# Kernel optimization log

Hardware: AMD Instinct MI355X
Metric: run time of the kernel (lower is better)

## Reference

```python
import math
import jax, jax.numpy as jnp
import numpy as np

EMBED_DIM = 512
NUM_HEADS = 8
PROJ_DIM = EMBED_DIM // NUM_HEADS
ATTN_WINDOW = 5
HALF_WINDOW = (ATTN_WINDOW - 1) // 2  # 2
ATTN_PARAM = 1.0
ATTN_DISPLACEMENT = 1
# per-head positions: ['center','left','right','center'] repeated to 8 heads (synst repeats short lists)
HEAD_SHIFTS = np.array([0, -ATTN_DISPLACEMENT, ATTN_DISPLACEMENT, 0] * 2, dtype=np.int32)


def _xavier(key, shape):
    fan_in, fan_out = shape[1], shape[0]
    bound = math.sqrt(6.0 / (fan_in + fan_out))
    return jax.random.uniform(key, shape, jnp.float32, -bound, bound)


def setup_inputs() -> dict:
    key = jax.random.key(0)
    k1, k2, k3, k4, k5 = jax.random.split(key, 5)
    B, S, E = 8, 4096, EMBED_DIM
    return {
        "values": jax.random.normal(k1, (B, S, E), jnp.float32),
        "keys": jax.random.normal(k2, (B, S, E), jnp.float32),
        "queries": jax.random.normal(k3, (B, S, E), jnp.float32),
        "input_weights": _xavier(k4, (E, E)),        # value projection (attn_weights=1, non-learned type)
        "out_proj_w": _xavier(k5, (E, E)),           # output_projection.weight (bias=False)
    }


def reference(values, keys, queries, input_weights, out_proj_w):
    # keys/queries are unused by the hard-coded 'normal' attention path (no QK^T)
    B, S, E = values.shape
    H, Dh, hw, W = NUM_HEADS, PROJ_DIM, HALF_WINDOW, ATTN_WINDOW

    # value projection + head split: [B,S,E] -> [B,H,S,Dh]
    v = values @ input_weights.T
    v = v.reshape(B, S, H, Dh).transpose(0, 2, 1, 3)

    # fixed Gaussian filter over relative distances [-hw, hw] (unnormalized pdf, as in the source)
    dist = jnp.arange(-hw, hw + 1, dtype=jnp.float32)
    filt = (1.0 / (ATTN_PARAM * math.sqrt(2.0 * math.pi))) * jnp.exp(-0.5 * (dist / ATTN_PARAM) ** 2)  # [W]

    shifts = jnp.asarray(HEAD_SHIFTS)            # [H] per-head center displacement
    P = hw + int(np.max(np.abs(HEAD_SHIFTS)))    # pad so all gathers are in range
    vp = jnp.pad(v, ((0, 0), (0, 0), (P, P), (0, 0)))  # [B,H,S+2P,Dh]

    h_ar = jnp.arange(H)[:, None]                # [H,1]
    pos = jnp.arange(S)[None, :]                 # [1,S]
    out = jnp.zeros_like(v)
    for j in range(W):                           # tiny fixed window loop (W=5)
        idx = pos + P + shifts[:, None] + (j - hw)   # [H,S]
        out = out + filt[j] * vp[:, h_ar, idx, :]    # [B,H,S,Dh]

    out = out.transpose(0, 2, 1, 3).reshape(B, S, E)
    return out @ out_proj_w.T
```

## Files before the change

kernel.cpp:

```cpp
#include <hip/hip_runtime.h>
#include <hip/hip_bf16.h>
#include <stdint.h>

typedef __bf16 bf16;
typedef __bf16 bf16x8 __attribute__((ext_vector_type(8)));
typedef float  f32x4  __attribute__((ext_vector_type(4)));

#define BM 128
#define BN 128
#define BK 64
#define E  512
#define SB 4112
#define M1 (8 * SB)
#define M2 32768

__device__ __forceinline__ void gl_lds_16(const bf16* g, bf16* l) {
    __builtin_amdgcn_global_load_lds(
        (__attribute__((address_space(1))) void*)g,
        (__attribute__((address_space(3))) void*)l,
        16, 0, 0);
}

__global__ __launch_bounds__(256)
void gemm_bt_bf16(const bf16* __restrict__ A, const bf16* __restrict__ Bm,
                  bf16* __restrict__ C, int M, int N, int K)
{
    __shared__ bf16 As[BM * BK];
    __shared__ bf16 Bs[BN * BK];

    const int tid  = threadIdx.x;
    const int id   = blockIdx.x;
    const int bm   = id >> 2;
    const int bn   = id & 3;
    const int wave = tid >> 6;
    const int lane = tid & 63;
    const int wm   = wave >> 1;
    const int wn   = wave & 1;

    const int srow = tid >> 3;
    const int scol = (((tid & 7) ^ (srow & 7)) << 3);
    const size_t a_off = (size_t)(bm * BM + srow) * K + scol;
    const size_t b_off = (size_t)(bn * BN + srow) * K + scol;
    const int    l_off = tid * 8;

    f32x4 acc[4][4] = {};
    const int fr = lane & 15;
    const int q  = lane >> 4;

    for (int k0 = 0; k0 < K; k0 += BK) {
#pragma unroll
        for (int c = 0; c < 4; ++c) {
            gl_lds_16(A  + a_off + (size_t)(c * 32) * K + k0, As + c * 2048 + l_off);
            gl_lds_16(Bm + b_off + (size_t)(c * 32) * K + k0, Bs + c * 2048 + l_off);
        }
        __syncthreads();

#pragma unroll
        for (int t = 0; t < 2; ++t) {
            bf16x8 af[4], bfr[4];
#pragma unroll
            for (int i = 0; i < 4; ++i) {
                const int Ra = wm * 64 + i * 16 + fr;
                const int Rb = wn * 64 + i * 16 + fr;
                const int c  = t * 4 + q;
                af[i]  = *(const bf16x8*)(As + Ra * BK + ((c ^ (Ra & 7)) << 3));
                bfr[i] = *(const bf16x8*)(Bs + Rb * BK + ((c ^ (Rb & 7)) << 3));
            }
#pragma unroll
            for (int i = 0; i < 4; ++i)
#pragma unroll
                for (int j = 0; j < 4; ++j)
                    acc[i][j] = __builtin_amdgcn_mfma_f32_16x16x32_bf16(af[i], bfr[j], acc[i][j], 0, 0, 0);
        }
        __syncthreads();
    }

    const int crow = (lane >> 4) << 2;
    const int ccol = lane & 15;
    const int row0 = bm * BM + wm * 64 + crow;
    const int col0 = bn * BN + wn * 64 + ccol;
#pragma unroll
    for (int i = 0; i < 4; ++i)
#pragma unroll
        for (int j = 0; j < 4; ++j)
#pragma unroll
            for (int r = 0; r < 4; ++r)
                C[(size_t)(row0 + i * 16 + r) * N + (col0 + j * 16)] = (bf16)acc[i][j][r];
}

__global__ __launch_bounds__(256)
void gemm2_gather(const bf16* __restrict__ P, const bf16* __restrict__ Bm,
                  float* __restrict__ C)
{
    __shared__ bf16 As[BM * BK];
    __shared__ bf16 Bs[BN * BK];

    const int tid  = threadIdx.x;
    const int id   = blockIdx.x;
    const int bm   = id >> 2;
    const int bn   = id & 3;
    const int wave = tid >> 6;
    const int lane = tid & 63;
    const int wm   = wave >> 1;
    const int wn   = wave & 1;

    const int srow = tid >> 3;
    const int scol = (((tid & 7) ^ (srow & 7)) << 3);
    const size_t b_off = (size_t)(bn * BN + srow) * E + scol;
    const int    l_off = tid * 8;

    f32x4 acc[4][4] = {};
    const int fr = lane & 15;
    const int q  = lane >> 4;

    for (int k0 = 0; k0 < E; k0 += BK) {
        const int h3 = (k0 >> 6) & 3;
        const int sh = (h3 == 1) ? -1 : (h3 == 2) ? 1 : 0;
#pragma unroll
        for (int c = 0; c < 4; ++c) {
            const int m = bm * BM + c * 32 + srow;
            const int prow = (m >> 12) * SB + (m & 4095) + 1 + sh;
            gl_lds_16(P  + (size_t)prow * E + k0 + scol,          As + c * 2048 + l_off);
            gl_lds_16(Bm + b_off + (size_t)(c * 32) * E + k0,     Bs + c * 2048 + l_off);
        }
        __syncthreads();

#pragma unroll
        for (int t = 0; t < 2; ++t) {
            bf16x8 af[4], bfr[4];
#pragma unroll
            for (int i = 0; i < 4; ++i) {
                const int Ra = wm * 64 + i * 16 + fr;
                const int Rb = wn * 64 + i * 16 + fr;
                const int c  = t * 4 + q;
                af[i]  = *(const bf16x8*)(As + Ra * BK + ((c ^ (Ra & 7)) << 3));
                bfr[i] = *(const bf16x8*)(Bs + Rb * BK + ((c ^ (Rb & 7)) << 3));
            }
#pragma unroll
            for (int i = 0; i < 4; ++i)
#pragma unroll
                for (int j = 0; j < 4; ++j)
                    acc[i][j] = __builtin_amdgcn_mfma_f32_16x16x32_bf16(af[i], bfr[j], acc[i][j], 0, 0, 0);
        }
        __syncthreads();
    }

    const int crow = (lane >> 4) << 2;
    const int ccol = lane & 15;
    const int row0 = bm * BM + wm * 64 + crow;
    const int col0 = bn * BN + wn * 64 + ccol;
#pragma unroll
    for (int i = 0; i < 4; ++i)
#pragma unroll
        for (int j = 0; j < 4; ++j)
#pragma unroll
            for (int r = 0; r < 4; ++r)
                C[(size_t)(row0 + i * 16 + r) * E + (col0 + j * 16)] = acc[i][j][r];
}

__global__ __launch_bounds__(256)
void prefilter(const float* __restrict__ vals, bf16* __restrict__ vg)
{
    const int tid  = threadIdx.x;
    const int e8   = tid & 63;
    const int gidx = blockIdx.x * 4 + (tid >> 6);
    const int m0   = gidx << 3;
    const int b    = m0 / SB;
    const int r0   = m0 - b * SB;

    const float filt[5] = {0.05399096651318806f, 0.24197072451914337f,
                           0.3989422804014327f,
                           0.24197072451914337f, 0.05399096651318806f};

    float acc[8][8];
#pragma unroll
    for (int t = 0; t < 8; ++t)
#pragma unroll
        for (int d = 0; d < 8; ++d) acc[t][d] = 0.f;

    const float* bbase = vals + (size_t)b * 4096 * E + e8 * 8;
#pragma unroll
    for (int u = 0; u < 12; ++u) {
        const int sp = r0 - 3 + u;
        if (sp >= 0 && sp < 4096) {
            const f32x4* p = (const f32x4*)(bbase + (size_t)sp * E);
            const f32x4 x0 = p[0], x1 = p[1];
            const float x[8] = {x0[0], x0[1], x0[2], x0[3],
                                x1[0], x1[1], x1[2], x1[3]};
#pragma unroll
            for (int t = 0; t < 8; ++t) {
                const int j = u - t;
                if (j >= 0 && j < 5) {
                    const float w = filt[j];
#pragma unroll
                    for (int d = 0; d < 8; ++d) acc[t][d] += w * x[d];
                }
            }
        }
    }
#pragma unroll
    for (int t = 0; t < 8; ++t) {
        bf16x8 o;
#pragma unroll
        for (int d = 0; d < 8; ++d) o[d] = (bf16)acc[t][d];
        *((bf16x8*)vg + (size_t)(m0 + t) * 64 + e8) = o;
    }
}

__global__ __launch_bounds__(256)
void cvt_weights(const float* __restrict__ w_in, const float* __restrict__ w_out,
                 bf16* __restrict__ win_b, bf16* __restrict__ wout_b)
{
    const int i = blockIdx.x * 256 + threadIdx.x;
    const int half = (E * E) / 8;
    const float* src = (i < half) ? w_in : w_out;
    bf16* dst        = (i < half) ? win_b : wout_b;
    const int k = (i < half) ? i : i - half;
    const f32x4* p = (const f32x4*)src + 2 * (size_t)k;
    f32x4 a = p[0], bq = p[1];
    bf16x8 o;
    o[0] = (bf16)a[0]; o[1] = (bf16)a[1]; o[2] = (bf16)a[2]; o[3] = (bf16)a[3];
    o[4] = (bf16)bq[0]; o[5] = (bf16)bq[1]; o[6] = (bf16)bq[2]; o[7] = (bf16)bq[3];
    *((bf16x8*)dst + k) = o;
}

extern "C" void kernel_launch(void* const* d_in, const int* in_sizes, int n_in,
                              void* d_out, int out_size, void* d_ws, size_t ws_size,
                              hipStream_t stream)
{
    const float* values = (const float*)d_in[0];
    const float* w_in   = (const float*)d_in[3];
    const float* w_out  = (const float*)d_in[4];
    float* out = (float*)d_out;

    bf16* win_b  = (bf16*)d_ws;
    bf16* wout_b = win_b + E * E;
    bf16* vg     = wout_b + E * E;
    bf16* Pbuf   = vg + (size_t)M1 * E;

    cvt_weights<<<(2 * E * E / 8) / 256, 256, 0, stream>>>(w_in, w_out, win_b, wout_b);
    prefilter<<<M1 / 8 / 4, 256, 0, stream>>>(values, vg);

    gemm_bt_bf16<<<(M1 / BM) * 4, 256, 0, stream>>>(vg, win_b, Pbuf, M1, E, E);
    gemm2_gather<<<(M2 / BM) * 4, 256, 0, stream>>>(Pbuf, wout_b, out);
}
```

Baseline: 242.4 us.

## Double-buffer larger-tile gather GEMM and fuse weight conversion into prefilter

The second GEMM moves to 256x256 tiles with 512 threads and double-buffered LDS, so the next K-slice loads while MFMAs run, and it raises wave priority around the compute. The weight conversion kernel is merged into the prefilter kernel through a block-index split, removing one launch. The larger tiles cut redundant global reads of the gathered P rows and the weights. In exchange the block uses 128KB of LDS and more accumulator registers, which limits occupancy.

```diff
diff --git a/kernel.cpp b/kernel.cpp
--- a/kernel.cpp
+++ b/kernel.cpp
@@ -88,69 +88,98 @@
                 C[(size_t)(row0 + i * 16 + r) * N + (col0 + j * 16)] = (bf16)acc[i][j][r];
 }
 
-__global__ __launch_bounds__(256)
+__global__ __launch_bounds__(512, 2)
 void gemm2_gather(const bf16* __restrict__ P, const bf16* __restrict__ Bm,
                   float* __restrict__ C)
 {
-    __shared__ bf16 As[BM * BK];
-    __shared__ bf16 Bs[BN * BK];
+    __shared__ bf16 As[2][256 * 64];
+    __shared__ bf16 Bs[2][256 * 64];
 
     const int tid  = threadIdx.x;
     const int id   = blockIdx.x;
-    const int bm   = id >> 2;
-    const int bn   = id & 3;
+    const int bm   = id >> 1;
+    const int bn   = id & 1;
     const int wave = tid >> 6;
     const int lane = tid & 63;
-    const int wm   = wave >> 1;
-    const int wn   = wave & 1;
+    const int wm   = wave >> 2;
+    const int wn   = wave & 3;
 
     const int srow = tid >> 3;
     const int scol = (((tid & 7) ^ (srow & 7)) << 3);
-    const size_t b_off = (size_t)(bn * BN + srow) * E + scol;
-    const int    l_off = tid * 8;
-
-    f32x4 acc[4][4] = {};
+    const int ldst = tid * 8;
+
+    f32x4 acc[8][4] = {};
     const int fr = lane & 15;
     const int q  = lane >> 4;
 
-    for (int k0 = 0; k0 < E; k0 += BK) {
-        const int h3 = (k0 >> 6) & 3;
+    auto stage = [&](int t, int p) {
+        const int k0 = t << 6;
+        const int h3 = t & 3;
         const int sh = (h3 == 1) ? -1 : (h3 == 2) ? 1 : 0;
 #pragma unroll
         for (int c = 0; c < 4; ++c) {
-            const int m = bm * BM + c * 32 + srow;
+            const int m    = bm * 256 + c * 64 + srow;
             const int prow = (m >> 12) * SB + (m & 4095) + 1 + sh;
-            gl_lds_16(P  + (size_t)prow * E + k0 + scol,          As + c * 2048 + l_off);
-            gl_lds_16(Bm + b_off + (size_t)(c * 32) * E + k0,     Bs + c * 2048 + l_off);
-        }
-        __syncthreads();
-
-#pragma unroll
-        for (int t = 0; t < 2; ++t) {
-            bf16x8 af[4], bfr[4];
-#pragma unroll
-            for (int i = 0; i < 4; ++i) {
-                const int Ra = wm * 64 + i * 16 + fr;
-                const int Rb = wn * 64 + i * 16 + fr;
-                const int c  = t * 4 + q;
-                af[i]  = *(const bf16x8*)(As + Ra * BK + ((c ^ (Ra & 7)) << 3));
-                bfr[i] = *(const bf16x8*)(Bs + Rb * BK + ((c ^ (Rb & 7)) << 3));
+            gl_lds_16(P + (size_t)prow * E + k0 + scol, &As[p][c * 4096 + ldst]);
+        }
+#pragma unroll
+        for (int c = 0; c < 4; ++c) {
+            const int n = bn * 256 + c * 64 + srow;
+            gl_lds_16(Bm + (size_t)n * E + k0 + scol, &Bs[p][c * 4096 + ldst]);
+        }
+    };
+
+    stage(0, 0);
+    __syncthreads();
+
+    for (int t = 0; t < 8; ++t) {
+        const int p = t & 1;
+        if (t < 7) stage(t + 1, p ^ 1);
+        __builtin_amdgcn_s_setprio(1);
+#pragma unroll
+        for (int ih = 0; ih < 2; ++ih) {
+            bf16x8 af[4][2];
+#pragma unroll
+            for (int ii = 0; ii < 4; ++ii)
+#pragma unroll
+                for (int ks = 0; ks < 2; ++ks) {
+                    const int Ra = wm * 128 + (ih * 4 + ii) * 16 + fr;
+                    const int ch = ks * 4 + q;
+                    af[ii][ks] = *(const bf16x8*)(&As[p][Ra * 64 + ((ch ^ (Ra & 7)) << 3)]);
+                }
+#pragma unroll
+            for (int jh = 0; jh < 2; ++jh) {
+                bf16x8 bfv[2][2];
+#pragma unroll
+                for (int jj = 0; jj < 2; ++jj)
+#pragma unroll
+                    for (int ks = 0; ks < 2; ++ks) {
+                        const int Rb = wn * 64 + (jh * 2 + jj) * 16 + fr;
+                        const int ch = ks * 4 + q;
+                        bfv[jj][ks] = *(const bf16x8*)(&Bs[p][Rb * 64 + ((ch ^ (Rb & 7)) << 3)]);
+                    }
+#pragma unroll
+                for (int ii = 0; ii < 4; ++ii)
+#pragma unroll
+                    for (int jj = 0; jj < 2; ++jj)
+#pragma unroll
+                        for (int ks = 0; ks < 2; ++ks)
+                            acc[ih * 4 + ii][jh * 2 + jj] =
+                                __builtin_amdgcn_mfma_f32_16x16x32_bf16(
+                                    af[ii][ks], bfv[jj][ks],
+                                    acc[ih * 4 + ii][jh * 2 + jj], 0, 0, 0);
             }
-#pragma unroll
-            for (int i = 0; i < 4; ++i)
-#pragma unroll
-                for (int j = 0; j < 4; ++j)
-                    acc[i][j] = __builtin_amdgcn_mfma_f32_16x16x32_bf16(af[i], bfr[j], acc[i][j], 0, 0, 0);
-        }
+        }
+        __builtin_amdgcn_s_setprio(0);
         __syncthreads();
     }
 
     const int crow = (lane >> 4) << 2;
     const int ccol = lane & 15;
-    const int row0 = bm * BM + wm * 64 + crow;
-    const int col0 = bn * BN + wn * 64 + ccol;
-#pragma unroll
-    for (int i = 0; i < 4; ++i)
+    const int row0 = bm * 256 + wm * 128 + crow;
+    const int col0 = bn * 256 + wn * 64 + ccol;
+#pragma unroll
+    for (int i = 0; i < 8; ++i)
 #pragma unroll
         for (int j = 0; j < 4; ++j)
 #pragma unroll
@@ -159,11 +188,30 @@
 }
 
 __global__ __launch_bounds__(256)
-void prefilter(const float* __restrict__ vals, bf16* __restrict__ vg)
-{
-    const int tid  = threadIdx.x;
+void prep(const float* __restrict__ vals, const float* __restrict__ w_in,
+          const float* __restrict__ w_out, bf16* __restrict__ vg,
+          bf16* __restrict__ win_b, bf16* __restrict__ wout_b)
+{
+    const int tid = threadIdx.x;
+    const int blk = blockIdx.x;
+
+    if (blk < 256) {
+        const int i = blk * 256 + tid;
+        const int half = (E * E) / 8;
+        const float* src = (i < half) ? w_in : w_out;
+        bf16* dst        = (i < half) ? win_b : wout_b;
+        const int k = (i < half) ? i : i - half;
+        const f32x4* p = (const f32x4*)src + 2 * (size_t)k;
+        f32x4 a = p[0], bq = p[1];
+        bf16x8 o;
+        o[0] = (bf16)a[0];  o[1] = (bf16)a[1];  o[2] = (bf16)a[2];  o[3] = (bf16)a[3];
+        o[4] = (bf16)bq[0]; o[5] = (bf16)bq[1]; o[6] = (bf16)bq[2]; o[7] = (bf16)bq[3];
+        *((bf16x8*)dst + k) = o;
+        return;
+    }
+
     const int e8   = tid & 63;
-    const int gidx = blockIdx.x * 4 + (tid >> 6);
+    const int gidx = (blk - 256) * 4 + (tid >> 6);
     const int m0   = gidx << 3;
     const int b    = m0 / SB;
     const int r0   = m0 - b * SB;
@@ -207,23 +255,6 @@
     }
 }
 
-__global__ __launch_bounds__(256)
-void cvt_weights(const float* __restrict__ w_in, const float* __restrict__ w_out,
-                 bf16* __restrict__ win_b, bf16* __restrict__ wout_b)
-{
-    const int i = blockIdx.x * 256 + threadIdx.x;
-    const int half = (E * E) / 8;
-    const float* src = (i < half) ? w_in : w_out;
-    bf16* dst        = (i < half) ? win_b : wout_b;
-    const int k = (i < half) ? i : i - half;
-    const f32x4* p = (const f32x4*)src + 2 * (size_t)k;
-    f32x4 a = p[0], bq = p[1];
-    bf16x8 o;
-    o[0] = (bf16)a[0]; o[1] = (bf16)a[1]; o[2] = (bf16)a[2]; o[3] = (bf16)a[3];
-    o[4] = (bf16)bq[0]; o[5] = (bf16)bq[1]; o[6] = (bf16)bq[2]; o[7] = (bf16)bq[3];
-    *((bf16x8*)dst + k) = o;
-}
-
 extern "C" void kernel_launch(void* const* d_in, const int* in_sizes, int n_in,
                               void* d_out, int out_size, void* d_ws, size_t ws_size,
                               hipStream_t stream)
@@ -238,9 +269,8 @@
     bf16* vg     = wout_b + E * E;
     bf16* Pbuf   = vg + (size_t)M1 * E;
 
-    cvt_weights<<<(2 * E * E / 8) / 256, 256, 0, stream>>>(w_in, w_out, win_b, wout_b);
-    prefilter<<<M1 / 8 / 4, 256, 0, stream>>>(values, vg);
+    prep<<<256 + M1 / 32, 256, 0, stream>>>(values, w_in, w_out, vg, win_b, wout_b);
 
     gemm_bt_bf16<<<(M1 / BM) * 4, 256, 0, stream>>>(vg, win_b, Pbuf, M1, E, E);
-    gemm2_gather<<<(M2 / BM) * 4, 256, 0, stream>>>(Pbuf, wout_b, out);
-}
+    gemm2_gather<<<(M2 / 256) * 2, 512, 0, stream>>>(Pbuf, wout_b, out);
+}
```

Measured after the change: 241.9 us. No clear change (-0.2%).
